# Kernel tuning notes

Measured on AMD Instinct MI355X. Metric: run time of the kernel, lower is better.

The kernel has to match this reference:

```python
import jax, jax.numpy as jnp
import numpy as np

N = 100_000   # nodes
E = 600_000   # edges per layer (avg degree ~6, ogbn-arxiv-like)
IN, H, C = 128, 256, 40


def _sage_layer(x, src, dst, w_self, w_neigh, b):
    """DGL SAGEConv with mean aggregator: fc_self(x) + fc_neigh(mean_nbr) + b."""
    n = x.shape[0]
    msg = x[src]                                               # [E, d] gather
    agg = jax.ops.segment_sum(msg, dst, num_segments=n)        # [N, d]
    deg = jax.ops.segment_sum(jnp.ones((src.shape[0],), x.dtype), dst,
                              num_segments=n)                  # [N]
    h_neigh = agg / jnp.maximum(deg, 1.0)[:, None]             # mean; 0 if isolated
    return x @ w_self.T + h_neigh @ w_neigh.T + b


def setup_inputs() -> dict:
    key = jax.random.key(0)
    ks = jax.random.split(key, 11)
    s = 0.02
    return {
        "x": jax.random.normal(ks[0], (N, IN), jnp.float32),
        "src1": jax.random.randint(ks[1], (E,), 0, N, jnp.int32),
        "dst1": jax.random.randint(ks[2], (E,), 0, N, jnp.int32),
        "src2": jax.random.randint(ks[3], (E,), 0, N, jnp.int32),
        "dst2": jax.random.randint(ks[4], (E,), 0, N, jnp.int32),
        "w_self1": s * jax.random.normal(ks[5], (H, IN), jnp.float32),
        "w_neigh1": s * jax.random.normal(ks[6], (H, IN), jnp.float32),
        "b1": jnp.zeros((H,), jnp.float32),
        "w_self2": s * jax.random.normal(ks[7], (C, H), jnp.float32),
        "w_neigh2": s * jax.random.normal(ks[8], (C, H), jnp.float32),
        "b2": jnp.zeros((C,), jnp.float32),
    }


def reference(x, src1, dst1, src2, dst2, w_self1, w_neigh1, b1,
              w_self2, w_neigh2, b2):
    h = jax.nn.relu(_sage_layer(x, src1, dst1, w_self1, w_neigh1, b1))
    return _sage_layer(h, src2, dst2, w_self2, w_neigh2, b2)
```

## Files before the change

kernel.cpp:

```cpp
#include <hip/hip_runtime.h>
#include <hip/hip_bf16.h>
#include <cstdint>
#include <cstddef>


#define D_IN 128
#define D_H  256
#define D_C  40

#define NBLK     128
#define NBKT_MAX 392
#define BKT_CAP  2560

typedef __bf16 bf16_t;
typedef __attribute__((ext_vector_type(8))) __bf16 bf16x8;
typedef __attribute__((ext_vector_type(4))) __bf16 bf16x4;
typedef __attribute__((ext_vector_type(4))) float  f32x4;

static constexpr size_t NMAX = 100000;
static constexpr size_t EMAX = 600000;
static constexpr size_t NSC_MAX = (size_t)NBKT_MAX * NBLK;
static constexpr size_t alignup(size_t v) { return (v + 255) & ~size_t(255); }

static constexpr size_t HG1_OFF  = 0;
static constexpr size_t HG2_OFF  = alignup(HG1_OFF + NSC_MAX * 4);
static constexpr size_t BS1_OFF  = alignup(HG2_OFF + NSC_MAX * 4);
static constexpr size_t BS2_OFF  = alignup(BS1_OFF + 512 * 4);
static constexpr size_t RP1_OFF  = alignup(BS2_OFF + 512 * 4);
static constexpr size_t RP2_OFF  = alignup(RP1_OFF + (NMAX + 1) * 4);
static constexpr size_t BKT1_OFF = alignup(RP2_OFF + (NMAX + 1) * 4);
static constexpr size_t BKT2_OFF = alignup(BKT1_OFF + EMAX * 4);
static constexpr size_t XCAT_OFF = alignup(BKT2_OFF + EMAX * 4);
static constexpr size_t P_OFF    = alignup(XCAT_OFF + (NMAX + 64) * 256 * 2);
static constexpr size_t W1F_OFF  = alignup(P_OFF + NMAX * 40 * 4);
static constexpr size_t W2F_OFF  = alignup(W1F_OFF + 32 * 256 * 8 * 2);
static constexpr size_t WS_NEEDED = W2F_OFF + 32 * 80 * 8 * 2;

__global__ __launch_bounds__(256) void k_prep(
    const float* __restrict__ x, bf16_t* __restrict__ xcat,
    const float* __restrict__ ws1, const float* __restrict__ wn1,
    const float* __restrict__ ws2, const float* __restrict__ wn2,
    bf16_t* __restrict__ w1f, bf16_t* __restrict__ w2f,
    const int* __restrict__ dst1, const int* __restrict__ dst2,
    int* __restrict__ hg1, int* __restrict__ hg2,
    int N, int E, int chunk, int nbkt, int nconvx) {
  __shared__ int h[NBKT_MAX];
  int bid = blockIdx.x;

  if (bid < nconvx) {
    int t = bid * 256 + threadIdx.x;
    if (t < N * 16) {
      int row = t >> 4, j = t & 15;
      const float* sp = x + (size_t)row * 128 + j * 8;
      float4 v0 = ((const float4*)sp)[0];
      float4 v1 = ((const float4*)sp)[1];
      bf16x8 o;
      o[0] = (bf16_t)v0.x; o[1] = (bf16_t)v0.y; o[2] = (bf16_t)v0.z; o[3] = (bf16_t)v0.w;
      o[4] = (bf16_t)v1.x; o[5] = (bf16_t)v1.y; o[6] = (bf16_t)v1.z; o[7] = (bf16_t)v1.w;
      *(bf16x8*)(xcat + (size_t)row * 256 + j * 8) = o;
    }
    return;
  }
  bid -= nconvx;

  if (bid < 32) {
    int t = bid * 256 + threadIdx.x;
    {
      int ks4g = t >> 8, col = t & 255;
      int k0 = (ks4g >> 2) * 32 + (ks4g & 3) * 8;
      bf16x8 o;
#pragma unroll
      for (int i = 0; i < 8; ++i) {
        int k = k0 + i;
        float v = (k < 128) ? ws1[col * 128 + k] : wn1[col * 128 + (k - 128)];
        o[i] = (bf16_t)v;
      }
      *(bf16x8*)(w1f + (size_t)t * 8) = o;
    }
    if (t < 32 * 80) {
      int ks4g = t / 80, col = t - ks4g * 80;
      int k0 = (ks4g >> 2) * 32 + (ks4g & 3) * 8;
      bf16x8 o;
#pragma unroll
      for (int i = 0; i < 8; ++i) {
        int k = k0 + i;
        float v = (col < 40) ? ws2[col * 256 + k] : wn2[(col - 40) * 256 + k];
        o[i] = (bf16_t)v;
      }
      *(bf16x8*)(w2f + (size_t)t * 8) = o;
    }
    return;
  }
  bid -= 32;
  {
    const int* dst = (bid >> 7) ? dst2 : dst1;
    int*       hg  = (bid >> 7) ? hg2 : hg1;
    int        cb  = bid & 127;
    for (int i = threadIdx.x; i < nbkt; i += 256) h[i] = 0;
    __syncthreads();
    int beg = cb * chunk, end = min(E, beg + chunk);
    for (int e = beg + threadIdx.x; e < end; e += 256)
      atomicAdd(&h[dst[e] >> 8], 1);
    __syncthreads();
    for (int b = threadIdx.x; b < nbkt; b += 256)
      hg[b * NBLK + cb] = h[b];
  }
}

__global__ void k_scan_block(int* __restrict__ a1, int* __restrict__ a2,
                             int* __restrict__ b1s, int* __restrict__ b2s, int n) {
  int* a    = blockIdx.y ? a2 : a1;
  int* bsum = blockIdx.y ? b2s : b1s;
  __shared__ int lds[256];
  int t = threadIdx.x, i = blockIdx.x * 256 + t;
  int v = (i < n) ? a[i] : 0;
  lds[t] = v;
  __syncthreads();
  for (int off = 1; off < 256; off <<= 1) {
    int add = (t >= off) ? lds[t - off] : 0;
    __syncthreads();
    lds[t] += add;
    __syncthreads();
  }
  if (i < n) a[i] = lds[t] - v;
  if (t == 255) bsum[blockIdx.x] = lds[255];
}

__global__ void k_scan_sums(int* __restrict__ b1s, int* __restrict__ b2s, int nb) {
  int* bsum = blockIdx.x ? b2s : b1s;
  __shared__ int lds[512];
  int t = threadIdx.x;
  int v = (t < nb) ? bsum[t] : 0;
  lds[t] = v;
  __syncthreads();
  for (int off = 1; off < 512; off <<= 1) {
    int add = (t >= off) ? lds[t - off] : 0;
    __syncthreads();
    lds[t] += add;
    __syncthreads();
  }
  if (t < nb) bsum[t] = lds[t] - v;
}

__global__ void k_scan_add(int* __restrict__ a1, int* __restrict__ a2,
                           const int* __restrict__ b1s, const int* __restrict__ b2s, int n) {
  int* a        = blockIdx.y ? a2 : a1;
  const int* bs = blockIdx.y ? b2s : b1s;
  int i = blockIdx.x * 256 + threadIdx.x;
  if (i < n) a[i] += bs[i >> 8];
}

__global__ void k_scat(const int* __restrict__ src1, const int* __restrict__ dst1,
                       const int* __restrict__ src2, const int* __restrict__ dst2,
                       const int* __restrict__ off1, const int* __restrict__ off2,
                       unsigned* __restrict__ bkt1, unsigned* __restrict__ bkt2,
                       int E, int chunk, int nbkt) {
  const int* src = blockIdx.y ? src2 : src1;
  const int* dst = blockIdx.y ? dst2 : dst1;
  const int* off = blockIdx.y ? off2 : off1;
  unsigned*  bkt = blockIdx.y ? bkt2 : bkt1;
  __shared__ int cur[NBKT_MAX];
  for (int i = threadIdx.x; i < nbkt; i += 256)
    cur[i] = off[i * NBLK + blockIdx.x];
  __syncthreads();
  int beg = blockIdx.x * chunk, end = min(E, beg + chunk);
  for (int e = beg + threadIdx.x; e < end; e += 256) {
    int d = dst[e];
    int slot = atomicAdd(&cur[d >> 8], 1);
    bkt[slot] = (unsigned)src[e] | ((unsigned)(d & 255) << 24);
  }
}

__global__ __launch_bounds__(256) void k_bcsr(
    const int* __restrict__ off1, const int* __restrict__ off2,
    const unsigned* bkt1, const unsigned* bkt2,
    int* csr1, int* csr2,
    int* __restrict__ rp1, int* __restrict__ rp2, int E, int N, int nbkt) {
  const int* off      = blockIdx.y ? off2 : off1;
  const unsigned* bkt = blockIdx.y ? bkt2 : bkt1;
  int* csr            = blockIdx.y ? csr2 : csr1;
  int* rowptr         = blockIdx.y ? rp2 : rp1;

  const int b = blockIdx.x, t = threadIdx.x;
  const int base = off[b * NBLK];
  const int endp = (b == nbkt - 1) ? E : off[(b + 1) * NBLK];
  const int cnt  = endp - base;

  __shared__ int hist[256];
  __shared__ int sc[256];
  __shared__ int cur[256];
  __shared__ int stage[BKT_CAP];

  hist[t] = 0;
  __syncthreads();
  for (int i = t; i < cnt; i += 256)
    atomicAdd(&hist[bkt[base + i] >> 24], 1);
  __syncthreads();

  int v = hist[t];
  sc[t] = v;
  __syncthreads();
  for (int off_ = 1; off_ < 256; off_ <<= 1) {
    int add = (t >= off_) ? sc[t - off_] : 0;
    __syncthreads();
    sc[t] += add;
    __syncthreads();
  }
  int excl = sc[t] - v;

  int node = b * 256 + t;
  if (node < N) rowptr[node] = base + excl;
  if (b == nbkt - 1 && t == 0) rowptr[N] = E;
  cur[t] = excl;
  __syncthreads();

  for (int i = t; i < cnt; i += 256) {
    unsigned u = bkt[base + i];
    int slot = atomicAdd(&cur[u >> 24], 1);
    if (slot < BKT_CAP) stage[slot] = (int)(u & 0xFFFFFFu);
  }
  __syncthreads();
  for (int i = t; i < cnt; i += 256)
    csr[base + i] = stage[i];
}

__global__ void k_agg1(bf16_t* __restrict__ xcat, const int* __restrict__ rowptr,
                       const int* __restrict__ csr, int N) {
  int t = blockIdx.x * 256 + threadIdx.x;
  int node = t >> 4, l = t & 15;
  if (node >= N) return;
  int beg = rowptr[node], end = rowptr[node + 1];
  float acc[8] = {0.f, 0.f, 0.f, 0.f, 0.f, 0.f, 0.f, 0.f};
  for (int e = beg; e < end; ++e) {
    int s = csr[e];
    bf16x8 v = *(const bf16x8*)(xcat + (size_t)s * 256 + l * 8);
#pragma unroll
    for (int i = 0; i < 8; ++i) acc[i] += (float)v[i];
  }
  float rd = (end > beg) ? 1.0f / (float)(end - beg) : 0.0f;
  bf16x8 o;
#pragma unroll
  for (int i = 0; i < 8; ++i) o[i] = (bf16_t)(acc[i] * rd);
  *(bf16x8*)(xcat + (size_t)node * 256 + 128 + l * 8) = o;
}

__global__ __launch_bounds__(256, 3) void k_fused(
    const bf16_t* __restrict__ xcat, const bf16_t* __restrict__ w1f,
    const float* __restrict__ b1, const bf16_t* __restrict__ w2f,
    const float* __restrict__ b2v, float* __restrict__ out,
    float* __restrict__ p, int N) {
  __shared__ __align__(16) char lds[32768];
  const int tid  = (int)threadIdx.x;
  const int wv   = tid >> 6;
  const int lane = tid & 63;
  const int lr   = lane & 15;
  const int lg   = lane >> 4;
  const int c0   = wv * 64;
  const int m0   = (int)blockIdx.x * 64;

  {
    const char* tb = (const char*)(xcat + (size_t)m0 * 256);
#pragma unroll
    for (int i = 0; i < 8; ++i) {
      int L   = i * 4096 + tid * 16;
      int row = L >> 9;
      int c   = L & 511;
      int so  = (row << 9) | (c ^ ((row & 7) << 4));
      __builtin_amdgcn_global_load_lds(
          (const __attribute__((address_space(1))) void*)(tb + so),
          (__attribute__((address_space(3))) void*)(lds + L), 16, 0, 0);
    }
  }
  __syncthreads();

  f32x4 acc[4][4] = {};
#pragma unroll
  for (int ks = 0; ks < 8; ++ks) {
    bf16x8 wf[4];
#pragma unroll
    for (int wb = 0; wb < 4; ++wb)
      wf[wb] = *(const bf16x8*)(w1f + ((size_t)(ks * 4 + lg) * 256 +
                                       (c0 + wb * 16 + lr)) * 8);
    bf16x8 ax[4];
#pragma unroll
    for (int rb = 0; rb < 4; ++rb) {
      int lrow = rb * 16 + lr;
      ax[rb] = *(const bf16x8*)(lds + lrow * 512 +
                                ((ks * 64 + lg * 16) ^ ((lrow & 7) << 4)));
    }
#pragma unroll
    for (int wb = 0; wb < 4; ++wb)
#pragma unroll
      for (int rb = 0; rb < 4; ++rb)
        acc[wb][rb] = __builtin_amdgcn_mfma_f32_16x16x32_bf16(
            wf[ks & 0 ? 0 : wb], ax[rb], acc[wb][rb], 0, 0, 0);
  }

  __syncthreads();

#pragma unroll
  for (int wb = 0; wb < 4; ++wb) {
    float4 b4 = *(const float4*)(b1 + c0 + wb * 16 + lg * 4);
#pragma unroll
    for (int rb = 0; rb < 4; ++rb) {
      int xrow = rb * 16 + lr;
      bf16x4 o;
      o[0] = (bf16_t)fmaxf(acc[wb][rb][0] + b4.x, 0.f);
      o[1] = (bf16_t)fmaxf(acc[wb][rb][1] + b4.y, 0.f);
      o[2] = (bf16_t)fmaxf(acc[wb][rb][2] + b4.z, 0.f);
      o[3] = (bf16_t)fmaxf(acc[wb][rb][3] + b4.w, 0.f);
      *(bf16x4*)(lds + xrow * 512 +
                 ((c0 * 2 + wb * 32 + lg * 8) ^ ((xrow & 7) << 4))) = o;
    }
  }
  __syncthreads();

  f32x4 acc2[5] = {};
  const int arow = wv * 16 + lr;
#pragma unroll
  for (int ks = 0; ks < 8; ++ks) {
    bf16x8 hf = *(const bf16x8*)(lds + arow * 512 +
                                 ((ks * 64 + lg * 16) ^ ((arow & 7) << 4)));
#pragma unroll
    for (int wb = 0; wb < 5; ++wb) {
      bf16x8 w2 = *(const bf16x8*)(w2f + ((size_t)(ks * 4 + lg) * 80 +
                                          (wb * 16 + lr)) * 8);
      acc2[wb] = __builtin_amdgcn_mfma_f32_16x16x32_bf16(
          w2, hf, acc2[wb], 0, 0, 0);
    }
  }

  const int r = m0 + wv * 16 + lr;
  if (r < N) {
#pragma unroll
    for (int wb = 0; wb < 5; ++wb) {
      int col0 = wb * 16 + lg * 4;
      f32x4 v = acc2[wb];
      if (col0 < 40) {
        float4 b4 = *(const float4*)(b2v + col0);
        v[0] += b4.x; v[1] += b4.y; v[2] += b4.z; v[3] += b4.w;
        *(f32x4*)(out + (size_t)r * 40 + col0) = v;
      } else {
        *(f32x4*)(p + (size_t)r * 40 + (col0 - 40)) = v;
      }
    }
  }
}

__global__ void k_agg2fin(const float* __restrict__ p, const int* __restrict__ rowptr,
                          const int* __restrict__ csr, float* __restrict__ out, int N) {
  int t = blockIdx.x * 256 + threadIdx.x;
  int node = t / 10, l = t - node * 10;
  if (node >= N) return;
  int beg = rowptr[node], end = rowptr[node + 1];
  float4 acc = {0.f, 0.f, 0.f, 0.f};
  for (int e = beg; e < end; ++e) {
    int s = csr[e];
    float4 v = *(const float4*)(p + (size_t)s * 40 + l * 4);
    acc.x += v.x; acc.y += v.y; acc.z += v.z; acc.w += v.w;
  }
  float rd = (end > beg) ? 1.0f / (float)(end - beg) : 0.0f;
  float* o = out + (size_t)node * 40 + l * 4;
  float4 cur = *(const float4*)o;
  cur.x += acc.x * rd;
  cur.y += acc.y * rd;
  cur.z += acc.z * rd;
  cur.w += acc.w * rd;
  *(float4*)o = cur;
}

extern "C" void kernel_launch(void* const* d_in, const int* in_sizes, int n_in,
                              void* d_out, int out_size, void* d_ws, size_t ws_size,
                              hipStream_t stream) {
  const float* x    = (const float*)d_in[0];
  const int*   src1 = (const int*)d_in[1];
  const int*   dst1 = (const int*)d_in[2];
  const int*   src2 = (const int*)d_in[3];
  const int*   dst2 = (const int*)d_in[4];
  const float* ws1  = (const float*)d_in[5];
  const float* wn1  = (const float*)d_in[6];
  const float* b1   = (const float*)d_in[7];
  const float* ws2  = (const float*)d_in[8];
  const float* wn2  = (const float*)d_in[9];
  const float* b2   = (const float*)d_in[10];
  float*       out  = (float*)d_out;

  const int N = in_sizes[0] / D_IN;
  const int E = in_sizes[1];
  if (ws_size < WS_NEEDED) return;

  char*     ws   = (char*)d_ws;
  int*      hg1  = (int*)(ws + HG1_OFF);
  int*      hg2  = (int*)(ws + HG2_OFF);
  int*      bs1  = (int*)(ws + BS1_OFF);
  int*      bs2  = (int*)(ws + BS2_OFF);
  int*      rp1  = (int*)(ws + RP1_OFF);
  int*      rp2  = (int*)(ws + RP2_OFF);
  unsigned* bkt1 = (unsigned*)(ws + BKT1_OFF);
  unsigned* bkt2 = (unsigned*)(ws + BKT2_OFF);
  int*      csr1 = (int*)(ws + BKT1_OFF);
  int*      csr2 = (int*)(ws + BKT2_OFF);
  bf16_t*   xcat = (bf16_t*)(ws + XCAT_OFF);
  float*    p    = (float*)(ws + P_OFF);
  bf16_t*   w1f  = (bf16_t*)(ws + W1F_OFF);
  bf16_t*   w2f  = (bf16_t*)(ws + W2F_OFF);

  const int nbkt  = (N + 255) >> 8;
  const int chunk = (E + NBLK - 1) / NBLK;
  const int nsc   = nbkt * NBLK;
  const int nscb  = (nsc + 255) / 256;
  const int nconvx = (N * 16 + 255) / 256;
  const int ntiles = (N + 63) / 64;

  k_prep<<<nconvx + 32 + 2 * NBLK, 256, 0, stream>>>(
      x, xcat, ws1, wn1, ws2, wn2, w1f, w2f, dst1, dst2, hg1, hg2,
      N, E, chunk, nbkt, nconvx);

  k_scan_block<<<dim3(nscb, 2), 256, 0, stream>>>(hg1, hg2, bs1, bs2, nsc);
  k_scan_sums<<<2, 512, 0, stream>>>(bs1, bs2, nscb);
  k_scan_add<<<dim3(nscb, 2), 256, 0, stream>>>(hg1, hg2, bs1, bs2, nsc);
  k_scat<<<dim3(NBLK, 2), 256, 0, stream>>>(src1, dst1, src2, dst2, hg1, hg2,
                                            bkt1, bkt2, E, chunk, nbkt);
  k_bcsr<<<dim3(nbkt, 2), 256, 0, stream>>>(hg1, hg2, bkt1, bkt2, csr1, csr2,
                                            rp1, rp2, E, N, nbkt);

  k_agg1<<<(N * 16 + 255) / 256, 256, 0, stream>>>(xcat, rp1, csr1, N);
  k_fused<<<ntiles, 256, 0, stream>>>(xcat, w1f, b1, w2f, b2, out, p, N);
  k_agg2fin<<<(N * 10 + 255) / 256, 256, 0, stream>>>(p, rp2, csr2, out, N);
}
```

Baseline: 159.0 us.

## Double fused GEMM row tile to 128 and store neighbor projection in bf16

The fused two-layer GEMM kernel now processes 128 rows per block instead of 64, so each weight fragment loaded from global memory feeds twice as many MFMAs. This needs 64KB of LDS and occupancy drops to 2 blocks per CU. The layer-2 neighbor projection buffer p is also stored as bf16 instead of fp32, halving the bytes gathered in the final aggregation, at some cost in precision. The xcat padding is widened to cover the larger tile.

New measurement: 153.0 us. 3.8% less time.

```diff
diff --git a/kernel.cpp b/kernel.cpp
--- a/kernel.cpp
+++ b/kernel.cpp
@@ -31,8 +31,8 @@
 static constexpr size_t BKT1_OFF = alignup(RP2_OFF + (NMAX + 1) * 4);
 static constexpr size_t BKT2_OFF = alignup(BKT1_OFF + EMAX * 4);
 static constexpr size_t XCAT_OFF = alignup(BKT2_OFF + EMAX * 4);
-static constexpr size_t P_OFF    = alignup(XCAT_OFF + (NMAX + 64) * 256 * 2);
-static constexpr size_t W1F_OFF  = alignup(P_OFF + NMAX * 40 * 4);
+static constexpr size_t P_OFF    = alignup(XCAT_OFF + (NMAX + 128) * 256 * 2);
+static constexpr size_t W1F_OFF  = alignup(P_OFF + NMAX * 40 * 2);
 static constexpr size_t W2F_OFF  = alignup(W1F_OFF + 32 * 256 * 8 * 2);
 static constexpr size_t WS_NEEDED = W2F_OFF + 32 * 80 * 8 * 2;
 
@@ -244,24 +244,24 @@
   *(bf16x8*)(xcat + (size_t)node * 256 + 128 + l * 8) = o;
 }
 
-__global__ __launch_bounds__(256, 3) void k_fused(
+__global__ __launch_bounds__(256, 2) void k_fused(
     const bf16_t* __restrict__ xcat, const bf16_t* __restrict__ w1f,
     const float* __restrict__ b1, const bf16_t* __restrict__ w2f,
     const float* __restrict__ b2v, float* __restrict__ out,
-    float* __restrict__ p, int N) {
-  __shared__ __align__(16) char lds[32768];
+    bf16_t* __restrict__ p, int N) {
+  __shared__ __align__(16) char lds[65536];
   const int tid  = (int)threadIdx.x;
   const int wv   = tid >> 6;
   const int lane = tid & 63;
   const int lr   = lane & 15;
   const int lg   = lane >> 4;
   const int c0   = wv * 64;
-  const int m0   = (int)blockIdx.x * 64;
+  const int m0   = (int)blockIdx.x * 128;
 
   {
     const char* tb = (const char*)(xcat + (size_t)m0 * 256);
 #pragma unroll
-    for (int i = 0; i < 8; ++i) {
+    for (int i = 0; i < 16; ++i) {
       int L   = i * 4096 + tid * 16;
       int row = L >> 9;
       int c   = L & 511;
@@ -273,7 +273,7 @@
   }
   __syncthreads();
 
-  f32x4 acc[4][4] = {};
+  f32x4 acc[4][8] = {};
 #pragma unroll
   for (int ks = 0; ks < 8; ++ks) {
     bf16x8 wf[4];
@@ -281,9 +281,9 @@
     for (int wb = 0; wb < 4; ++wb)
       wf[wb] = *(const bf16x8*)(w1f + ((size_t)(ks * 4 + lg) * 256 +
                                        (c0 + wb * 16 + lr)) * 8);
-    bf16x8 ax[4];
-#pragma unroll
-    for (int rb = 0; rb < 4; ++rb) {
+    bf16x8 ax[8];
+#pragma unroll
+    for (int rb = 0; rb < 8; ++rb) {
       int lrow = rb * 16 + lr;
       ax[rb] = *(const bf16x8*)(lds + lrow * 512 +
                                 ((ks * 64 + lg * 16) ^ ((lrow & 7) << 4)));
@@ -291,9 +291,9 @@
 #pragma unroll
     for (int wb = 0; wb < 4; ++wb)
 #pragma unroll
-      for (int rb = 0; rb < 4; ++rb)
+      for (int rb = 0; rb < 8; ++rb)
         acc[wb][rb] = __builtin_amdgcn_mfma_f32_16x16x32_bf16(
-            wf[ks & 0 ? 0 : wb], ax[rb], acc[wb][rb], 0, 0, 0);
+            wf[wb], ax[rb], acc[wb][rb], 0, 0, 0);
   }
 
   __syncthreads();
@@ -302,7 +302,7 @@
   for (int wb = 0; wb < 4; ++wb) {
     float4 b4 = *(const float4*)(b1 + c0 + wb * 16 + lg * 4);
 #pragma unroll
-    for (int rb = 0; rb < 4; ++rb) {
+    for (int rb = 0; rb < 8; ++rb) {
       int xrow = rb * 16 + lr;
       bf16x4 o;
       o[0] = (bf16_t)fmaxf(acc[wb][rb][0] + b4.x, 0.f);
@@ -315,57 +315,69 @@
   }
   __syncthreads();
 
-  f32x4 acc2[5] = {};
-  const int arow = wv * 16 + lr;
+  f32x4 acc2[2][5] = {};
 #pragma unroll
   for (int ks = 0; ks < 8; ++ks) {
-    bf16x8 hf = *(const bf16x8*)(lds + arow * 512 +
-                                 ((ks * 64 + lg * 16) ^ ((arow & 7) << 4)));
+    bf16x8 hf[2];
+#pragma unroll
+    for (int m = 0; m < 2; ++m) {
+      int arow = wv * 32 + m * 16 + lr;
+      hf[m] = *(const bf16x8*)(lds + arow * 512 +
+                               ((ks * 64 + lg * 16) ^ ((arow & 7) << 4)));
+    }
 #pragma unroll
     for (int wb = 0; wb < 5; ++wb) {
       bf16x8 w2 = *(const bf16x8*)(w2f + ((size_t)(ks * 4 + lg) * 80 +
                                           (wb * 16 + lr)) * 8);
-      acc2[wb] = __builtin_amdgcn_mfma_f32_16x16x32_bf16(
-          w2, hf, acc2[wb], 0, 0, 0);
-    }
-  }
-
-  const int r = m0 + wv * 16 + lr;
-  if (r < N) {
-#pragma unroll
-    for (int wb = 0; wb < 5; ++wb) {
-      int col0 = wb * 16 + lg * 4;
-      f32x4 v = acc2[wb];
-      if (col0 < 40) {
-        float4 b4 = *(const float4*)(b2v + col0);
-        v[0] += b4.x; v[1] += b4.y; v[2] += b4.z; v[3] += b4.w;
-        *(f32x4*)(out + (size_t)r * 40 + col0) = v;
-      } else {
-        *(f32x4*)(p + (size_t)r * 40 + (col0 - 40)) = v;
+#pragma unroll
+      for (int m = 0; m < 2; ++m)
+        acc2[m][wb] = __builtin_amdgcn_mfma_f32_16x16x32_bf16(
+            w2, hf[m], acc2[m][wb], 0, 0, 0);
+    }
+  }
+
+#pragma unroll
+  for (int m = 0; m < 2; ++m) {
+    const int r = m0 + wv * 32 + m * 16 + lr;
+    if (r < N) {
+#pragma unroll
+      for (int wb = 0; wb < 5; ++wb) {
+        int col0 = wb * 16 + lg * 4;
+        f32x4 v = acc2[m][wb];
+        if (col0 < 40) {
+          float4 b4 = *(const float4*)(b2v + col0);
+          v[0] += b4.x; v[1] += b4.y; v[2] += b4.z; v[3] += b4.w;
+          *(f32x4*)(out + (size_t)r * 40 + col0) = v;
+        } else {
+          bf16x4 o;
+          o[0] = (bf16_t)v[0]; o[1] = (bf16_t)v[1];
+          o[2] = (bf16_t)v[2]; o[3] = (bf16_t)v[3];
+          *(bf16x4*)(p + (size_t)r * 40 + (col0 - 40)) = o;
+        }
       }
     }
   }
 }
 
-__global__ void k_agg2fin(const float* __restrict__ p, const int* __restrict__ rowptr,
+__global__ void k_agg2fin(const bf16_t* __restrict__ p, const int* __restrict__ rowptr,
                           const int* __restrict__ csr, float* __restrict__ out, int N) {
   int t = blockIdx.x * 256 + threadIdx.x;
   int node = t / 10, l = t - node * 10;
   if (node >= N) return;
   int beg = rowptr[node], end = rowptr[node + 1];
-  float4 acc = {0.f, 0.f, 0.f, 0.f};
+  float a0 = 0.f, a1 = 0.f, a2 = 0.f, a3 = 0.f;
   for (int e = beg; e < end; ++e) {
     int s = csr[e];
-    float4 v = *(const float4*)(p + (size_t)s * 40 + l * 4);
-    acc.x += v.x; acc.y += v.y; acc.z += v.z; acc.w += v.w;
+    bf16x4 v = *(const bf16x4*)(p + (size_t)s * 40 + l * 4);
+    a0 += (float)v[0]; a1 += (float)v[1]; a2 += (float)v[2]; a3 += (float)v[3];
   }
   float rd = (end > beg) ? 1.0f / (float)(end - beg) : 0.0f;
   float* o = out + (size_t)node * 40 + l * 4;
   float4 cur = *(const float4*)o;
-  cur.x += acc.x * rd;
-  cur.y += acc.y * rd;
-  cur.z += acc.z * rd;
-  cur.w += acc.w * rd;
+  cur.x += a0 * rd;
+  cur.y += a1 * rd;
+  cur.z += a2 * rd;
+  cur.w += a3 * rd;
   *(float4*)o = cur;
 }
 
@@ -401,7 +413,7 @@
   int*      csr1 = (int*)(ws + BKT1_OFF);
   int*      csr2 = (int*)(ws + BKT2_OFF);
   bf16_t*   xcat = (bf16_t*)(ws + XCAT_OFF);
-  float*    p    = (float*)(ws + P_OFF);
+  bf16_t*   p    = (bf16_t*)(ws + P_OFF);
   bf16_t*   w1f  = (bf16_t*)(ws + W1F_OFF);
   bf16_t*   w2f  = (bf16_t*)(ws + W2F_OFF);
 
@@ -410,7 +422,7 @@
   const int nsc   = nbkt * NBLK;
   const int nscb  = (nsc + 255) / 256;
   const int nconvx = (N * 16 + 255) / 256;
-  const int ntiles = (N + 63) / 64;
+  const int ntiles = (N + 127) / 128;
 
   k_prep<<<nconvx + 32 + 2 * NBLK, 256, 0, stream>>>(
       x, xcat, ws1, wn1, ws2, wn2, w1f, w2f, dst1, dst2, hg1, hg2,
```
